# Kernel optimization log

Hardware: AMD Instinct MI355X
Metric: run time of the kernel (lower is better)

The kernel has to match this reference:

```python
import jax, jax.numpy as jnp
import numpy as np

B, S, D, H, F = 4, 2048, 1024, 16, 2048
DK = D // H
EPS = 1e-5


def layernorm(x, g, b):
    mu = jnp.mean(x, axis=-1, keepdims=True)
    var = jnp.mean(jnp.square(x - mu), axis=-1, keepdims=True)
    return (x - mu) * jax.lax.rsqrt(var + EPS) * g + b


def setup_inputs() -> dict:
    key = jax.random.key(0)
    ks = jax.random.split(key, 16)
    s = 0.02
    inp = {
        "src_representations_batch": jax.random.normal(ks[0], (B, S, D), jnp.float32),
        "src_mask": jnp.ones((B, 1, 1, S), dtype=bool),
        "wq": jax.random.normal(ks[1], (D, D), jnp.float32) * s,
        "bq": jnp.zeros((D,), jnp.float32),
        "wk": jax.random.normal(ks[2], (D, D), jnp.float32) * s,
        "bk": jnp.zeros((D,), jnp.float32),
        "wv": jax.random.normal(ks[3], (D, D), jnp.float32) * s,
        "bv": jnp.zeros((D,), jnp.float32),
        "wo": jax.random.normal(ks[4], (D, D), jnp.float32) * s,
        "bo": jnp.zeros((D,), jnp.float32),
        "ln1_g": jnp.ones((D,), jnp.float32),
        "ln1_b": jnp.zeros((D,), jnp.float32),
        "ln2_g": jnp.ones((D,), jnp.float32),
        "ln2_b": jnp.zeros((D,), jnp.float32),
        "w1": jax.random.normal(ks[5], (D, F), jnp.float32) * s,
        "b1": jnp.zeros((F,), jnp.float32),
        "w2": jax.random.normal(ks[6], (F, D), jnp.float32) * s,
        "b2": jnp.zeros((D,), jnp.float32),
    }
    return inp


def reference(src_representations_batch, src_mask, wq, bq, wk, bk, wv, bv, wo, bo,
              ln1_g, ln1_b, ln2_g, ln2_b, w1, b1, w2, b2):
    x = src_representations_batch
    # sublayer 1: x + MHA(LN(x))   (dropout is identity at inference)
    h = layernorm(x, ln1_g, ln1_b)  # [B,S,D]
    q = (h @ wq + bq).reshape(B, S, H, DK).transpose(0, 2, 1, 3)  # [B,H,S,DK]
    k = (h @ wk + bk).reshape(B, S, H, DK).transpose(0, 2, 1, 3)
    v = (h @ wv + bv).reshape(B, S, H, DK).transpose(0, 2, 1, 3)
    scores = jnp.einsum("bhqd,bhkd->bhqk", q, k) / jnp.sqrt(jnp.float32(DK))
    scores = jnp.where(src_mask, scores, jnp.float32(-jnp.inf))
    attn = jax.nn.softmax(scores, axis=-1)
    ctx = jnp.einsum("bhqk,bhkd->bhqd", attn, v)  # [B,H,S,DK]
    ctx = ctx.transpose(0, 2, 1, 3).reshape(B, S, D)
    x = x + (ctx @ wo + bo)
    # sublayer 2: x + FFN(LN(x))
    h2 = layernorm(x, ln2_g, ln2_b)
    ff = jax.nn.relu(h2 @ w1 + b1) @ w2 + b2
    return x + ff
```

## Files before the change

### kernel.cpp

```cpp
#include <hip/hip_runtime.h>
#include <hip/hip_bf16.h>
#include <cstdint>
#include <cstddef>

typedef __attribute__((ext_vector_type(8))) __bf16 bf16x8;
typedef __attribute__((ext_vector_type(4))) __bf16 bf16x4;
typedef __attribute__((ext_vector_type(4))) float f32x4;
typedef __attribute__((ext_vector_type(16))) float f32x16;

constexpr int SEQ = 2048, DIM = 1024, NB = 4, NH = 16, HD = 64, FFD = 2048;
constexpr int MR = NB * SEQ;
constexpr int QKVN = 3 * DIM;
#define QSCALE 0.18033688011112042f

#define AS1 __attribute__((address_space(1)))
#define AS3 __attribute__((address_space(3)))

__device__ __forceinline__ void gload_lds16(const void* g, void* l) {
  __builtin_amdgcn_global_load_lds((const AS1 void*)g, (AS3 void*)l, 16, 0, 0);
}

__device__ __forceinline__ float exp2x(float x) {
#if __has_builtin(__builtin_amdgcn_exp2f)
  return __builtin_amdgcn_exp2f(x);
#else
  return exp2f(x);
#endif
}

__device__ __forceinline__ uint32_t cvtpk(float lo, float hi) {
  uint32_t r;
  asm("v_cvt_pk_bf16_f32 %0, %1, %2" : "=v"(r) : "v"(lo), "v"(hi));
  return r;
}

__device__ __forceinline__ void pl32swap(uint32_t& a, uint32_t& b) {
  asm volatile("v_permlane32_swap_b32 %0, %1" : "+v"(a), "+v"(b));
}

__device__ __forceinline__ void memfence() { asm volatile("" ::: "memory"); }

__global__ __launch_bounds__(256) void transpose_cast(const float* __restrict__ W,
                                                      __bf16* __restrict__ Wt,
                                                      int K, int N, float scale) {
  __shared__ float tile[32][33];
  const int bk = blockIdx.y * 32, bn = blockIdx.x * 32;
  const int t = threadIdx.x;
  const int r = t >> 5, c = t & 31;
#pragma unroll
  for (int p = 0; p < 4; ++p)
    tile[r + p * 8][c] = W[(size_t)(bk + r + p * 8) * N + bn + c];
  __syncthreads();
#pragma unroll
  for (int p = 0; p < 4; ++p)
    Wt[(size_t)(bn + r + p * 8) * K + bk + c] = (__bf16)(tile[c][r + p * 8] * scale);
}

__global__ __launch_bounds__(256) void bias_fuse(const float* __restrict__ bq,
                                                 const float* __restrict__ bk,
                                                 const float* __restrict__ bv,
                                                 float* __restrict__ o) {
  const int i = blockIdx.x * 256 + threadIdx.x;
  o[i] = (i < DIM) ? bq[i] * QSCALE : (i < 2 * DIM ? bk[i - DIM] : bv[i - 2 * DIM]);
}

__global__ __launch_bounds__(256) void vtrans_kernel(const __bf16* __restrict__ V,
                                                     __bf16* __restrict__ Vt, int ldv) {
  __shared__ float tile[32][33];
  const int t = threadIdx.x;
  const int r = t >> 3, c4 = (t & 7) * 4;
  const int gr = blockIdx.y * 32;
  const int gc = blockIdx.x * 32;
  bf16x4 v = *(const bf16x4*)(V + (size_t)(gr + r) * ldv + gc + c4);
#pragma unroll
  for (int j = 0; j < 4; ++j) tile[r][c4 + j] = (float)v[j];
  __syncthreads();
  const int b = blockIdx.y >> 6;
  const int s0 = (blockIdx.y & 63) * 32;
  const int drow = gc + r;
  bf16x4 o;
#pragma unroll
  for (int j = 0; j < 4; ++j) o[j] = (__bf16)tile[c4 + j][r];
  *(bf16x4*)(Vt + ((size_t)b * NH * HD + drow) * SEQ + s0 + c4) = o;
}

__global__ __launch_bounds__(256) void ln_kernel(const float* __restrict__ x,
                                                 const float* __restrict__ g,
                                                 const float* __restrict__ b,
                                                 __bf16* __restrict__ out) {
  const int row = blockIdx.x;
  const int t = threadIdx.x;
  const float4 v = ((const float4*)(x + (size_t)row * DIM))[t];
  float s = v.x + v.y + v.z + v.w;
  float ss = v.x * v.x + v.y * v.y + v.z * v.z + v.w * v.w;
#pragma unroll
  for (int off = 32; off; off >>= 1) {
    s += __shfl_down(s, off);
    ss += __shfl_down(ss, off);
  }
  __shared__ float red[10];
  const int wave = t >> 6, lane = t & 63;
  if (lane == 0) { red[wave] = s; red[4 + wave] = ss; }
  __syncthreads();
  if (t == 0) {
    float S = red[0] + red[1] + red[2] + red[3];
    float SS = red[4] + red[5] + red[6] + red[7];
    float mu = S * (1.0f / DIM);
    float var = SS * (1.0f / DIM) - mu * mu;
    red[8] = mu;
    red[9] = rsqrtf(var + 1e-5f);
  }
  __syncthreads();
  const float mu = red[8], ri = red[9];
  const float4 gv = ((const float4*)g)[t];
  const float4 bv = ((const float4*)b)[t];
  bf16x4 o;
  o[0] = (__bf16)((v.x - mu) * ri * gv.x + bv.x);
  o[1] = (__bf16)((v.y - mu) * ri * gv.y + bv.y);
  o[2] = (__bf16)((v.z - mu) * ri * gv.z + bv.z);
  o[3] = (__bf16)((v.w - mu) * ri * gv.w + bv.w);
  *(bf16x4*)(out + (size_t)row * DIM + t * 4) = o;
}

template <bool RELU, bool ADD_RES, bool OUT_BF16>
__global__ __launch_bounds__(512, 2) void gemm_bt(const __bf16* __restrict__ A,
                                                  const __bf16* __restrict__ Bt,
                                                  const float* __restrict__ bias,
                                                  const float* __restrict__ resid,
                                                  void* __restrict__ Cout,
                                                  int M, int N, int K, float bscale) {
  __shared__ __bf16 lds[3][24576];
  const int t = threadIdx.x;
  const int wave = t >> 6, lane = t & 63;
  const int lr = lane & 15, l4 = lane >> 4;
  const int wr = wave >> 2, wc = wave & 3;
  const int gx = gridDim.x, nwg = gx * gridDim.y;
  const int hw = blockIdx.y * gx + blockIdx.x;
  const int lgid = (hw & 7) * (nwg >> 3) + (hw >> 3);
  const int m0 = (lgid / gx) * 128, n0 = (lgid % gx) * 256;
  const int NKT = K >> 6;

  auto stage = [&](int kt, __bf16* base) {
    const int k0 = kt << 6;
    const int row = t >> 3, cc = (t & 7) ^ (row & 7);
    gload_lds16(A + (size_t)(m0 + row) * K + k0 + cc * 8,
                base + (size_t)(wave * 64) * 8);
    gload_lds16(A + (size_t)(m0 + 64 + row) * K + k0 + cc * 8,
                base + 4096 + (size_t)(wave * 64) * 8);
#pragma unroll
    for (int j = 0; j < 4; ++j) {
      const int c = j * 512 + t;
      const int br = c >> 3, bc = (c & 7) ^ (br & 7);
      gload_lds16(Bt + (size_t)(n0 + br) * K + k0 + bc * 8,
                  base + 8192 + (size_t)(j * 512 + wave * 64) * 8);
    }
  };

  __bf16* pc = lds[0];
  __bf16* pn = lds[1];
  __bf16* p2 = lds[2];

  stage(0, pc);
  stage(1, pn);
  asm volatile("s_waitcnt vmcnt(6)" ::: "memory");
  __builtin_amdgcn_s_barrier();
  memfence();

  f32x4 acc[4][4] = {};

  for (int kt = 0; kt < NKT; ++kt) {
    if (kt + 2 < NKT) stage(kt + 2, p2);

    bf16x8 af[4][2], bfr[4][2];
#pragma unroll
    for (int mi = 0; mi < 4; ++mi)
#pragma unroll
      for (int ks = 0; ks < 2; ++ks) {
        const int row = wr * 64 + mi * 16 + lr;
        af[mi][ks] = *(const bf16x8*)(pc + row * 64 + (((ks * 4 + l4) ^ (row & 7)) * 8));
      }
#pragma unroll
    for (int nj = 0; nj < 4; ++nj)
#pragma unroll
      for (int ks = 0; ks < 2; ++ks) {
        const int row = wc * 64 + nj * 16 + lr;
        bfr[nj][ks] = *(const bf16x8*)(pc + 8192 + row * 64 + (((ks * 4 + l4) ^ (row & 7)) * 8));
      }

    __builtin_amdgcn_s_setprio(1);
#pragma unroll
    for (int mi = 0; mi < 4; ++mi)
#pragma unroll
      for (int nj = 0; nj < 4; ++nj)
#pragma unroll
        for (int ks = 0; ks < 2; ++ks)
          acc[mi][nj] = __builtin_amdgcn_mfma_f32_16x16x32_bf16(af[mi][ks], bfr[nj][ks], acc[mi][nj], 0, 0, 0);
    __builtin_amdgcn_s_setprio(0);

    if (kt + 2 < NKT) { asm volatile("s_waitcnt vmcnt(6)" ::: "memory"); }
    else              { asm volatile("s_waitcnt vmcnt(0)" ::: "memory"); }
    __builtin_amdgcn_s_barrier();
    memfence();
    __bf16* tmp = pc; pc = pn; pn = p2; p2 = tmp;
  }

  const int rb0 = l4 * 4;
#pragma unroll
  for (int nj = 0; nj < 4; ++nj) {
    const int col = n0 + wc * 64 + nj * 16 + lr;
    const float bc = bias[col] * bscale;
#pragma unroll
    for (int mi = 0; mi < 4; ++mi) {
#pragma unroll
      for (int r = 0; r < 4; ++r) {
        const int row = m0 + wr * 64 + mi * 16 + rb0 + r;
        float v = acc[mi][nj][r] + bc;
        if (RELU) v = fmaxf(v, 0.0f);
        if (ADD_RES) v += resid[(size_t)row * N + col];
        if (OUT_BF16)
          ((__bf16*)Cout)[(size_t)row * N + col] = (__bf16)v;
        else
          ((float*)Cout)[(size_t)row * N + col] = v;
      }
    }
  }
}

__global__ __launch_bounds__(256, 4) void attn_kernel(const __bf16* __restrict__ Q,
                                                      const __bf16* __restrict__ Kb,
                                                      const __bf16* __restrict__ Vt,
                                                      __bf16* __restrict__ ctx, int ld) {
  __shared__ __bf16 sK[2][64 * 64];
  __shared__ __bf16 sV[2][64 * 64];
  const int t = threadIdx.x;
  const int wave = t >> 6, lane = t & 63;
  const int l31 = lane & 31, hi = lane >> 5;
  const int swz = l31 & 7;
  const int nwg = gridDim.x;
  const int hw = blockIdx.x;
  const int lid = (hw & 7) * (nwg >> 3) + (hw >> 3);
  const int qb = lid & 15, h = (lid >> 4) & 15, b = lid >> 8;
  const size_t baseq = (size_t)b * SEQ * ld + (size_t)h * HD;
  const size_t basec = (size_t)b * SEQ * DIM + (size_t)h * HD;
  const size_t vtbase = ((size_t)b * NH + h) * (size_t)HD * SEQ;
  const int q0 = qb * 128 + wave * 32;

  bf16x8 qf[4];
#pragma unroll
  for (int ks = 0; ks < 4; ++ks)
    qf[ks] = *(const bf16x8*)(Q + baseq + (size_t)(q0 + l31) * ld + ks * 16 + hi * 8);

  bf16x8 onesf;
#pragma unroll
  for (int j = 0; j < 8; ++j) onesf[j] = (__bf16)1.0f;

  f32x16 acc[2] = {};
  f32x16 lacc = {};

  auto stage = [&](int kb, int buf) {
#pragma unroll
    for (int i = 0; i < 2; ++i) {
      const int c = i * 256 + wave * 64 + lane;
      const int kr = c >> 3, kc = (c & 7) ^ (kr & 7);
      gload_lds16(Kb + baseq + (size_t)(kb * 64 + kr) * ld + kc * 8,
                  &sK[buf][(size_t)(i * 256 + wave * 64) * 8]);
      gload_lds16(Vt + vtbase + (size_t)kr * SEQ + kb * 64 + kc * 8,
                  &sV[buf][(size_t)(i * 256 + wave * 64) * 8]);
    }
  };

  stage(0, 0);
  __syncthreads();

  constexpr int NT = SEQ / 64;
  int cur = 0;
  for (int kb = 0; kb < NT; ++kb) {
    if (kb + 1 < NT) stage(kb + 1, cur ^ 1);
    const __bf16* bK = sK[cur];
    const __bf16* bV = sV[cur];

    f32x16 sc[2] = {};
#pragma unroll
    for (int kn = 0; kn < 2; ++kn) {
#pragma unroll
      for (int ks = 0; ks < 4; ++ks) {
        const bf16x8 kf = *(const bf16x8*)(bK + (size_t)(kn * 32 + l31) * 64 +
                                           (((ks * 2 + hi) ^ swz) * 8));
        sc[kn] = __builtin_amdgcn_mfma_f32_32x32x16_bf16(kf, qf[ks], sc[kn], 0, 0, 0);
      }
    }

#pragma unroll
    for (int s = 0; s < 4; ++s) {
      const int kn = s >> 1, s1 = s & 1;
      bf16x8 vf[2];
#pragma unroll
      for (int dn = 0; dn < 2; ++dn)
        vf[dn] = *(const bf16x8*)(bV + (size_t)(dn * 32 + l31) * 64 +
                                  (((s * 2 + hi) ^ swz) * 8));
      uint32_t w0 = cvtpk(exp2x(sc[kn][8 * s1 + 0]), exp2x(sc[kn][8 * s1 + 1]));
      uint32_t w1 = cvtpk(exp2x(sc[kn][8 * s1 + 2]), exp2x(sc[kn][8 * s1 + 3]));
      uint32_t w2 = cvtpk(exp2x(sc[kn][8 * s1 + 4]), exp2x(sc[kn][8 * s1 + 5]));
      uint32_t w3 = cvtpk(exp2x(sc[kn][8 * s1 + 6]), exp2x(sc[kn][8 * s1 + 7]));
      pl32swap(w0, w2);
      pl32swap(w1, w3);
      union { uint32_t u[4]; bf16x8 v; } pa;
      pa.u[0] = w0; pa.u[1] = w1; pa.u[2] = w2; pa.u[3] = w3;
      acc[0] = __builtin_amdgcn_mfma_f32_32x32x16_bf16(pa.v, vf[0], acc[0], 0, 0, 0);
      acc[1] = __builtin_amdgcn_mfma_f32_32x32x16_bf16(pa.v, vf[1], acc[1], 0, 0, 0);
      lacc   = __builtin_amdgcn_mfma_f32_32x32x16_bf16(pa.v, onesf, lacc, 0, 0, 0);
    }
    __syncthreads();
    cur ^= 1;
  }

#pragma unroll
  for (int r = 0; r < 16; ++r) {
    const int q31 = (r & 3) + 8 * (r >> 2) + 4 * hi;
    const float ir = 1.0f / lacc[r];
    const size_t row = q0 + q31;
#pragma unroll
    for (int dn = 0; dn < 2; ++dn)
      ctx[basec + row * DIM + dn * 32 + l31] = (__bf16)(acc[dn][r] * ir);
  }
}

extern "C" void kernel_launch(void* const* d_in, const int* in_sizes, int n_in,
                              void* d_out, int out_size, void* d_ws, size_t ws_size,
                              hipStream_t stream) {
  (void)in_sizes; (void)n_in; (void)out_size; (void)ws_size;
  const float* x   = (const float*)d_in[0];
  const float* wq  = (const float*)d_in[2];
  const float* bq  = (const float*)d_in[3];
  const float* wk  = (const float*)d_in[4];
  const float* bk  = (const float*)d_in[5];
  const float* wv  = (const float*)d_in[6];
  const float* bv  = (const float*)d_in[7];
  const float* wo  = (const float*)d_in[8];
  const float* bo  = (const float*)d_in[9];
  const float* g1  = (const float*)d_in[10];
  const float* be1 = (const float*)d_in[11];
  const float* g2  = (const float*)d_in[12];
  const float* be2 = (const float*)d_in[13];
  const float* w1  = (const float*)d_in[14];
  const float* b1  = (const float*)d_in[15];
  const float* w2  = (const float*)d_in[16];
  const float* b2  = (const float*)d_in[17];
  float* out = (float*)d_out;

  char* ws = (char*)d_ws;
  size_t off = 0;
  auto alloc = [&](size_t bytes) -> char* {
    char* p = ws + off;
    off += (bytes + 255) & ~(size_t)255;
    return p;
  };
  __bf16* wqkvt = (__bf16*)alloc((size_t)QKVN * DIM * 2);
  __bf16* wot   = (__bf16*)alloc((size_t)DIM * DIM * 2);
  __bf16* w1t   = (__bf16*)alloc((size_t)DIM * FFD * 2);
  __bf16* w2t   = (__bf16*)alloc((size_t)FFD * DIM * 2);
  float*  qkvb  = (float*)alloc((size_t)QKVN * 4);
  __bf16* hbuf  = (__bf16*)alloc((size_t)MR * DIM * 2);
  __bf16* qkv   = (__bf16*)alloc((size_t)MR * QKVN * 2);
  __bf16* ctx   = (__bf16*)alloc((size_t)MR * DIM * 2);
  __bf16* vtb   = hbuf;
  __bf16* h2    = hbuf;
  __bf16* fbuf  = qkv;
  float*  x2    = (float*)d_out;

  const dim3 blk(256);
  const dim3 gblk(512);
  transpose_cast<<<dim3(DIM / 32, DIM / 32), blk, 0, stream>>>(wq, wqkvt, DIM, DIM, QSCALE);
  transpose_cast<<<dim3(DIM / 32, DIM / 32), blk, 0, stream>>>(wk, wqkvt + (size_t)DIM * DIM, DIM, DIM, 1.0f);
  transpose_cast<<<dim3(DIM / 32, DIM / 32), blk, 0, stream>>>(wv, wqkvt + (size_t)2 * DIM * DIM, DIM, DIM, 1.0f);
  transpose_cast<<<dim3(DIM / 32, DIM / 32), blk, 0, stream>>>(wo, wot, DIM, DIM, 1.0f);
  transpose_cast<<<dim3(FFD / 32, DIM / 32), blk, 0, stream>>>(w1, w1t, DIM, FFD, 1.0f);
  transpose_cast<<<dim3(DIM / 32, FFD / 32), blk, 0, stream>>>(w2, w2t, FFD, DIM, 1.0f);
  bias_fuse<<<dim3(QKVN / 256), blk, 0, stream>>>(bq, bk, bv, qkvb);

  ln_kernel<<<MR, blk, 0, stream>>>(x, g1, be1, hbuf);
  gemm_bt<false, false, true><<<dim3(QKVN / 256, MR / 128), gblk, 0, stream>>>(
      hbuf, wqkvt, qkvb, nullptr, qkv, MR, QKVN, DIM, 1.0f);
  vtrans_kernel<<<dim3(DIM / 32, MR / 32), blk, 0, stream>>>(qkv + 2 * DIM, vtb, QKVN);
  attn_kernel<<<dim3(NB * NH * (SEQ / 128)), blk, 0, stream>>>(qkv, qkv + DIM, vtb, ctx, QKVN);
  gemm_bt<false, true, false><<<dim3(DIM / 256, MR / 128), gblk, 0, stream>>>(
      ctx, wot, bo, x, x2, MR, DIM, DIM, 1.0f);

  ln_kernel<<<MR, blk, 0, stream>>>(x2, g2, be2, h2);
  gemm_bt<true, false, true><<<dim3(FFD / 256, MR / 128), gblk, 0, stream>>>(
      h2, w1t, b1, nullptr, fbuf, MR, FFD, DIM, 1.0f);
  gemm_bt<false, true, false><<<dim3(DIM / 256, MR / 128), gblk, 0, stream>>>(
      fbuf, w2t, b2, x2, out, MR, DIM, FFD, 1.0f);
}
```

Baseline: 291.2 us.

## Add 256x256 GEMM kernel, split QKV projection, change LDS swizzle and add setprio

Adds a new gemm256 kernel with 256x256 output tiles, double-buffered 64-wide K tiles and a two-level XOR swizzle, and uses it for the QK projection and the FFN up-projection. The fused QKV GEMM becomes a QK GEMM plus a separate V GEMM on the old kernel, so V gets its own contiguous buffer for the transpose. The attention kernel switches to the new swizzle and raises wave priority around its MFMA blocks. Larger tiles are meant to raise data reuse per workgroup, at the cost of fewer workgroups (occupancy and tail risk) and an extra kernel launch for V.

```diff
diff --git a/kernel.cpp b/kernel.cpp
--- a/kernel.cpp
+++ b/kernel.cpp
@@ -10,7 +10,7 @@
 
 constexpr int SEQ = 2048, DIM = 1024, NB = 4, NH = 16, HD = 64, FFD = 2048;
 constexpr int MR = NB * SEQ;
-constexpr int QKVN = 3 * DIM;
+constexpr int QKN = 2 * DIM;
 #define QSCALE 0.18033688011112042f
 
 #define AS1 __attribute__((address_space(1)))
@@ -40,6 +40,8 @@
 
 __device__ __forceinline__ void memfence() { asm volatile("" ::: "memory"); }
 
+__device__ __forceinline__ int swzr(int row) { return (row & 7) ^ ((row >> 3) & 7); }
+
 __global__ __launch_bounds__(256) void transpose_cast(const float* __restrict__ W,
                                                       __bf16* __restrict__ Wt,
                                                       int K, int N, float scale) {
@@ -56,12 +58,11 @@
     Wt[(size_t)(bn + r + p * 8) * K + bk + c] = (__bf16)(tile[c][r + p * 8] * scale);
 }
 
-__global__ __launch_bounds__(256) void bias_fuse(const float* __restrict__ bq,
-                                                 const float* __restrict__ bk,
-                                                 const float* __restrict__ bv,
-                                                 float* __restrict__ o) {
+__global__ __launch_bounds__(256) void bias_fuse2(const float* __restrict__ bq,
+                                                  const float* __restrict__ bk,
+                                                  float* __restrict__ o) {
   const int i = blockIdx.x * 256 + threadIdx.x;
-  o[i] = (i < DIM) ? bq[i] * QSCALE : (i < 2 * DIM ? bk[i - DIM] : bv[i - 2 * DIM]);
+  o[i] = (i < DIM) ? bq[i] * QSCALE : bk[i - DIM];
 }
 
 __global__ __launch_bounds__(256) void vtrans_kernel(const __bf16* __restrict__ V,
@@ -123,6 +124,101 @@
 }
 
 template <bool RELU, bool ADD_RES, bool OUT_BF16>
+__global__ __launch_bounds__(512, 2) void gemm256(const __bf16* __restrict__ A,
+                                                  const __bf16* __restrict__ Bt,
+                                                  const float* __restrict__ bias,
+                                                  const float* __restrict__ resid,
+                                                  void* __restrict__ Cout,
+                                                  int M, int N, int K, float bscale) {
+  __shared__ __bf16 lds[2][32768];
+  const int t = threadIdx.x;
+  const int wave = t >> 6, lane = t & 63;
+  const int lr = lane & 15, l4 = lane >> 4;
+  const int wr = wave >> 2, wc = wave & 3;
+  const int gx = gridDim.x, nwg = gx * gridDim.y;
+  const int hw = blockIdx.y * gx + blockIdx.x;
+  const int lgid = (hw & 7) * (nwg >> 3) + (hw >> 3);
+  const int m0 = (lgid / gx) * 256, n0 = (lgid % gx) * 256;
+  const int NKT = K >> 6;
+
+  auto stage = [&](int kt, int buf) {
+    const int k0 = kt << 6;
+    __bf16* base = lds[buf];
+#pragma unroll
+    for (int j = 0; j < 4; ++j) {
+      const int c = j * 512 + t;
+      const int row = c >> 3, cc = (c & 7) ^ swzr(row);
+      gload_lds16(A + (size_t)(m0 + row) * K + k0 + cc * 8,
+                  base + (size_t)(j * 512 + wave * 64) * 8);
+      gload_lds16(Bt + (size_t)(n0 + row) * K + k0 + cc * 8,
+                  base + 16384 + (size_t)(j * 512 + wave * 64) * 8);
+    }
+  };
+
+  stage(0, 0);
+  asm volatile("s_waitcnt vmcnt(0)" ::: "memory");
+  __builtin_amdgcn_s_barrier();
+  memfence();
+
+  f32x4 acc[8][4] = {};
+
+  int cur = 0;
+  for (int kt = 0; kt < NKT; ++kt) {
+    if (kt + 1 < NKT) stage(kt + 1, cur ^ 1);
+    const __bf16* bb = lds[cur];
+    bf16x8 bf[4][2];
+#pragma unroll
+    for (int nj = 0; nj < 4; ++nj)
+#pragma unroll
+      for (int ks = 0; ks < 2; ++ks) {
+        const int row = wc * 64 + nj * 16 + lr;
+        bf[nj][ks] = *(const bf16x8*)(bb + 16384 + row * 64 + (((ks * 4 + l4) ^ swzr(row)) * 8));
+      }
+#pragma unroll
+    for (int mi = 0; mi < 8; ++mi) {
+      bf16x8 af[2];
+#pragma unroll
+      for (int ks = 0; ks < 2; ++ks) {
+        const int row = wr * 128 + mi * 16 + lr;
+        af[ks] = *(const bf16x8*)(bb + row * 64 + (((ks * 4 + l4) ^ swzr(row)) * 8));
+      }
+      __builtin_amdgcn_s_setprio(1);
+#pragma unroll
+      for (int nj = 0; nj < 4; ++nj)
+#pragma unroll
+        for (int ks = 0; ks < 2; ++ks)
+          acc[mi][nj] = __builtin_amdgcn_mfma_f32_16x16x32_bf16(af[ks], bf[nj][ks], acc[mi][nj], 0, 0, 0);
+      __builtin_amdgcn_s_setprio(0);
+    }
+    asm volatile("s_waitcnt vmcnt(0)" ::: "memory");
+    __builtin_amdgcn_s_barrier();
+    memfence();
+    cur ^= 1;
+  }
+
+  const int rb0 = l4 * 4;
+#pragma unroll
+  for (int nj = 0; nj < 4; ++nj) {
+    const int col = n0 + wc * 64 + nj * 16 + lr;
+    const float bc = bias[col] * bscale;
+#pragma unroll
+    for (int mi = 0; mi < 8; ++mi) {
+#pragma unroll
+      for (int r = 0; r < 4; ++r) {
+        const int row = m0 + wr * 128 + mi * 16 + rb0 + r;
+        float v = acc[mi][nj][r] + bc;
+        if (RELU) v = fmaxf(v, 0.0f);
+        if (ADD_RES) v += resid[(size_t)row * N + col];
+        if (OUT_BF16)
+          ((__bf16*)Cout)[(size_t)row * N + col] = (__bf16)v;
+        else
+          ((float*)Cout)[(size_t)row * N + col] = v;
+      }
+    }
+  }
+}
+
+template <bool RELU, bool ADD_RES, bool OUT_BF16>
 __global__ __launch_bounds__(512, 2) void gemm_bt(const __bf16* __restrict__ A,
                                                   const __bf16* __restrict__ Bt,
                                                   const float* __restrict__ bias,
@@ -235,7 +331,6 @@
   const int t = threadIdx.x;
   const int wave = t >> 6, lane = t & 63;
   const int l31 = lane & 31, hi = lane >> 5;
-  const int swz = l31 & 7;
   const int nwg = gridDim.x;
   const int hw = blockIdx.x;
   const int lid = (hw & 7) * (nwg >> 3) + (hw >> 3);
@@ -261,7 +356,7 @@
 #pragma unroll
     for (int i = 0; i < 2; ++i) {
       const int c = i * 256 + wave * 64 + lane;
-      const int kr = c >> 3, kc = (c & 7) ^ (kr & 7);
+      const int kr = c >> 3, kc = (c & 7) ^ swzr(kr);
       gload_lds16(Kb + baseq + (size_t)(kb * 64 + kr) * ld + kc * 8,
                   &sK[buf][(size_t)(i * 256 + wave * 64) * 8]);
       gload_lds16(Vt + vtbase + (size_t)kr * SEQ + kb * 64 + kc * 8,
@@ -282,12 +377,15 @@
     f32x16 sc[2] = {};
 #pragma unroll
     for (int kn = 0; kn < 2; ++kn) {
+      const int row = kn * 32 + l31;
+      const int sw = swzr(row);
+      __builtin_amdgcn_s_setprio(1);
 #pragma unroll
       for (int ks = 0; ks < 4; ++ks) {
-        const bf16x8 kf = *(const bf16x8*)(bK + (size_t)(kn * 32 + l31) * 64 +
-                                           (((ks * 2 + hi) ^ swz) * 8));
+        const bf16x8 kf = *(const bf16x8*)(bK + (size_t)row * 64 + (((ks * 2 + hi) ^ sw) * 8));
         sc[kn] = __builtin_amdgcn_mfma_f32_32x32x16_bf16(kf, qf[ks], sc[kn], 0, 0, 0);
       }
+      __builtin_amdgcn_s_setprio(0);
     }
 
 #pragma unroll
@@ -295,9 +393,10 @@
       const int kn = s >> 1, s1 = s & 1;
       bf16x8 vf[2];
 #pragma unroll
-      for (int dn = 0; dn < 2; ++dn)
-        vf[dn] = *(const bf16x8*)(bV + (size_t)(dn * 32 + l31) * 64 +
-                                  (((s * 2 + hi) ^ swz) * 8));
+      for (int dn = 0; dn < 2; ++dn) {
+        const int row = dn * 32 + l31;
+        vf[dn] = *(const bf16x8*)(bV + (size_t)row * 64 + (((s * 2 + hi) ^ swzr(row)) * 8));
+      }
       uint32_t w0 = cvtpk(exp2x(sc[kn][8 * s1 + 0]), exp2x(sc[kn][8 * s1 + 1]));
       uint32_t w1 = cvtpk(exp2x(sc[kn][8 * s1 + 2]), exp2x(sc[kn][8 * s1 + 3]));
       uint32_t w2 = cvtpk(exp2x(sc[kn][8 * s1 + 4]), exp2x(sc[kn][8 * s1 + 5]));
@@ -306,9 +405,11 @@
       pl32swap(w1, w3);
       union { uint32_t u[4]; bf16x8 v; } pa;
       pa.u[0] = w0; pa.u[1] = w1; pa.u[2] = w2; pa.u[3] = w3;
+      __builtin_amdgcn_s_setprio(1);
       acc[0] = __builtin_amdgcn_mfma_f32_32x32x16_bf16(pa.v, vf[0], acc[0], 0, 0, 0);
       acc[1] = __builtin_amdgcn_mfma_f32_32x32x16_bf16(pa.v, vf[1], acc[1], 0, 0, 0);
       lacc   = __builtin_amdgcn_mfma_f32_32x32x16_bf16(pa.v, onesf, lacc, 0, 0, 0);
+      __builtin_amdgcn_s_setprio(0);
     }
     __syncthreads();
     cur ^= 1;
@@ -355,39 +456,43 @@
     off += (bytes + 255) & ~(size_t)255;
     return p;
   };
-  __bf16* wqkvt = (__bf16*)alloc((size_t)QKVN * DIM * 2);
-  __bf16* wot   = (__bf16*)alloc((size_t)DIM * DIM * 2);
-  __bf16* w1t   = (__bf16*)alloc((size_t)DIM * FFD * 2);
-  __bf16* w2t   = (__bf16*)alloc((size_t)FFD * DIM * 2);
-  float*  qkvb  = (float*)alloc((size_t)QKVN * 4);
-  __bf16* hbuf  = (__bf16*)alloc((size_t)MR * DIM * 2);
-  __bf16* qkv   = (__bf16*)alloc((size_t)MR * QKVN * 2);
-  __bf16* ctx   = (__bf16*)alloc((size_t)MR * DIM * 2);
-  __bf16* vtb   = hbuf;
-  __bf16* h2    = hbuf;
-  __bf16* fbuf  = qkv;
-  float*  x2    = (float*)d_out;
+  __bf16* wqkt = (__bf16*)alloc((size_t)QKN * DIM * 2);
+  __bf16* wvt  = (__bf16*)alloc((size_t)DIM * DIM * 2);
+  __bf16* wot  = (__bf16*)alloc((size_t)DIM * DIM * 2);
+  __bf16* w1t  = (__bf16*)alloc((size_t)DIM * FFD * 2);
+  __bf16* w2t  = (__bf16*)alloc((size_t)FFD * DIM * 2);
+  float*  qkb  = (float*)alloc((size_t)QKN * 4);
+  __bf16* hbuf = (__bf16*)alloc((size_t)MR * DIM * 2);
+  __bf16* qk   = (__bf16*)alloc((size_t)MR * QKN * 2);
+  __bf16* vbuf = (__bf16*)alloc((size_t)MR * DIM * 2);
+  __bf16* fbuf = (__bf16*)alloc((size_t)MR * FFD * 2);
+  __bf16* vtb  = hbuf;
+  __bf16* ctx  = vbuf;
+  __bf16* h2   = qk;
+  float*  x2   = (float*)d_out;
 
   const dim3 blk(256);
   const dim3 gblk(512);
-  transpose_cast<<<dim3(DIM / 32, DIM / 32), blk, 0, stream>>>(wq, wqkvt, DIM, DIM, QSCALE);
-  transpose_cast<<<dim3(DIM / 32, DIM / 32), blk, 0, stream>>>(wk, wqkvt + (size_t)DIM * DIM, DIM, DIM, 1.0f);
-  transpose_cast<<<dim3(DIM / 32, DIM / 32), blk, 0, stream>>>(wv, wqkvt + (size_t)2 * DIM * DIM, DIM, DIM, 1.0f);
+  transpose_cast<<<dim3(DIM / 32, DIM / 32), blk, 0, stream>>>(wq, wqkt, DIM, DIM, QSCALE);
+  transpose_cast<<<dim3(DIM / 32, DIM / 32), blk, 0, stream>>>(wk, wqkt + (size_t)DIM * DIM, DIM, DIM, 1.0f);
+  transpose_cast<<<dim3(DIM / 32, DIM / 32), blk, 0, stream>>>(wv, wvt, DIM, DIM, 1.0f);
   transpose_cast<<<dim3(DIM / 32, DIM / 32), blk, 0, stream>>>(wo, wot, DIM, DIM, 1.0f);
   transpose_cast<<<dim3(FFD / 32, DIM / 32), blk, 0, stream>>>(w1, w1t, DIM, FFD, 1.0f);
   transpose_cast<<<dim3(DIM / 32, FFD / 32), blk, 0, stream>>>(w2, w2t, FFD, DIM, 1.0f);
-  bias_fuse<<<dim3(QKVN / 256), blk, 0, stream>>>(bq, bk, bv, qkvb);
+  bias_fuse2<<<dim3(QKN / 256), blk, 0, stream>>>(bq, bk, qkb);
 
   ln_kernel<<<MR, blk, 0, stream>>>(x, g1, be1, hbuf);
-  gemm_bt<false, false, true><<<dim3(QKVN / 256, MR / 128), gblk, 0, stream>>>(
-      hbuf, wqkvt, qkvb, nullptr, qkv, MR, QKVN, DIM, 1.0f);
-  vtrans_kernel<<<dim3(DIM / 32, MR / 32), blk, 0, stream>>>(qkv + 2 * DIM, vtb, QKVN);
-  attn_kernel<<<dim3(NB * NH * (SEQ / 128)), blk, 0, stream>>>(qkv, qkv + DIM, vtb, ctx, QKVN);
+  gemm256<false, false, true><<<dim3(QKN / 256, MR / 256), gblk, 0, stream>>>(
+      hbuf, wqkt, qkb, nullptr, qk, MR, QKN, DIM, 1.0f);
+  gemm_bt<false, false, true><<<dim3(DIM / 256, MR / 128), gblk, 0, stream>>>(
+      hbuf, wvt, bv, nullptr, vbuf, MR, DIM, DIM, 1.0f);
+  vtrans_kernel<<<dim3(DIM / 32, MR / 32), blk, 0, stream>>>(vbuf, vtb, DIM);
+  attn_kernel<<<dim3(NB * NH * (SEQ / 128)), blk, 0, stream>>>(qk, qk + DIM, vtb, ctx, QKN);
   gemm_bt<false, true, false><<<dim3(DIM / 256, MR / 128), gblk, 0, stream>>>(
       ctx, wot, bo, x, x2, MR, DIM, DIM, 1.0f);
 
   ln_kernel<<<MR, blk, 0, stream>>>(x2, g2, be2, h2);
-  gemm_bt<true, false, true><<<dim3(FFD / 256, MR / 128), gblk, 0, stream>>>(
+  gemm256<true, false, true><<<dim3(FFD / 256, MR / 256), gblk, 0, stream>>>(
       h2, w1t, b1, nullptr, fbuf, MR, FFD, DIM, 1.0f);
   gemm_bt<false, true, false><<<dim3(DIM / 256, MR / 128), gblk, 0, stream>>>(
       fbuf, w2t, b2, x2, out, MR, DIM, FFD, 1.0f);
```

Result: slower. 308.3 us (+5.9%).
